# Kernel optimization log

Hardware: AMD Instinct MI355X
Metric: run time of the kernel (lower is better)

## Reference

```python
import math
import jax, jax.numpy as jnp
import numpy as np

B, S, HID = 4, 2048, 1024
H, D = 16, 64  # num_head, head_dim
EPS = 1e-12  # F.normalize eps


def _qknorm(t, gamma):
    # t: [B, S, H, D]; F.normalize(dim=-1) * sqrt(D) * gamma[None]
    norm = jnp.sqrt(jnp.sum(t * t, axis=-1, keepdims=True))
    t = t / jnp.maximum(norm, EPS)
    return t * math.sqrt(D) * gamma  # gamma broadcasts over [B,S]


def setup_inputs() -> dict:
    key = jax.random.key(0)
    ks = jax.random.split(key, 8)
    s = 0.02
    return {
        "x": jax.random.normal(ks[0], (B, S, HID), jnp.float32),
        "q_w": jax.random.normal(ks[1], (HID, HID), jnp.float32) * s,
        "q_b": jnp.zeros((HID,), jnp.float32),
        "kv_w": jax.random.normal(ks[2], (2 * HID, HID), jnp.float32) * s,
        "kv_b": jnp.zeros((2 * HID,), jnp.float32),
        "gamma_q": jnp.ones((H, D), jnp.float32),
        "gamma_k": jnp.ones((H, D), jnp.float32),
        "out_w": jax.random.normal(ks[3], (HID, HID), jnp.float32) * s,
    }


def reference(x, q_w, q_b, kv_w, kv_b, gamma_q, gamma_k, out_w):
    # self-attention: context = x
    q = (x @ q_w.T + q_b).reshape(B, S, H, D)
    kv = x @ kv_w.T + kv_b  # [B, S, 2*HID]
    k, v = jnp.split(kv, 2, axis=-1)
    k = k.reshape(B, S, H, D)
    v = v.reshape(B, S, H, D)
    q = _qknorm(q, gamma_q)
    k = _qknorm(k, gamma_k)
    scores = jnp.einsum('bqhd,bkhd->bhqk', q, k)  # [B,H,S,S]
    attn = jax.nn.softmax(scores, axis=-1)
    out = jnp.einsum('bhqk,bkhd->bqhd', attn, v).reshape(B, S, HID)
    return out @ out_w.T
```

## Files before the change

### kernel.cpp

```cpp
#include <hip/hip_runtime.h>
#include <stdint.h>

#define B_ 4
#define S_ 2048
#define HID_ 1024
#define NH_ 16
#define HD_ 64

typedef __bf16 bf16x8 __attribute__((ext_vector_type(8)));
typedef __bf16 bf16x4 __attribute__((ext_vector_type(4)));
typedef float f32x4 __attribute__((ext_vector_type(4)));

__device__ inline void gload_lds16(const void* g, void* l) {
  __builtin_amdgcn_global_load_lds((const __attribute__((address_space(1))) unsigned int*)g,
                                   (__attribute__((address_space(3))) unsigned int*)l, 16, 0, 0);
}

__device__ inline f32x4 fmax4(f32x4 a, f32x4 b) {
  f32x4 r;
  r[0] = fmaxf(a[0], b[0]); r[1] = fmaxf(a[1], b[1]);
  r[2] = fmaxf(a[2], b[2]); r[3] = fmaxf(a[3], b[3]);
  return r;
}

__global__ __launch_bounds__(256) void cvt_bf16(const float* __restrict__ in, __bf16* __restrict__ out) {
  int i = (blockIdx.x * 256 + threadIdx.x) * 4;
  f32x4 v = *(const f32x4*)(in + i);
  bf16x4 o;
  o[0] = (__bf16)v[0]; o[1] = (__bf16)v[1]; o[2] = (__bf16)v[2]; o[3] = (__bf16)v[3];
  *(bf16x4*)(out + i) = o;
}

template <int MODE>
__global__ __launch_bounds__(256) void gemm_bt(const __bf16* __restrict__ A,
                                               const __bf16* __restrict__ Bt,
                                               const float* __restrict__ bias_q,
                                               const float* __restrict__ bias_kv,
                                               const float* __restrict__ gamma_q,
                                               const float* __restrict__ gamma_k,
                                               __bf16* __restrict__ Cq,
                                               __bf16* __restrict__ Ck,
                                               float* __restrict__ Cf,
                                               __bf16* __restrict__ vt,
                                               int M, int N, int K) {
  const int n0 = blockIdx.x * 128;
  const int m0 = blockIdx.y * 128;
  const int tid  = threadIdx.x;
  const int wave = tid >> 6, lane = tid & 63;
  const int wm = wave >> 1, wn = wave & 1;
  const int lrow = lane & 15, lgrp = lane >> 4;

  __shared__ __bf16 sA[128][64];
  __shared__ __bf16 sB[128][64];

  f32x4 acc[4][4];
#pragma unroll
  for (int i = 0; i < 4; i++)
#pragma unroll
    for (int j = 0; j < 4; j++) acc[i][j] = f32x4{0.f, 0.f, 0.f, 0.f};

  for (int k0 = 0; k0 < K; k0 += 64) {
    __syncthreads();
#pragma unroll
    for (int c = 0; c < 4; c++) {
      const int row = wave * 32 + c * 8;
      const __bf16* ga = A + (size_t)(m0 + row + (lane >> 3)) * K + k0 + (lane & 7) * 8;
      gload_lds16(ga, &sA[row][0]);
      const __bf16* gb = Bt + (size_t)(n0 + row + (lane >> 3)) * K + k0 + (lane & 7) * 8;
      gload_lds16(gb, &sB[row][0]);
    }
    __syncthreads();
#pragma unroll
    for (int kk = 0; kk < 2; kk++) {
      bf16x8 af[4], bfr[4];
#pragma unroll
      for (int i = 0; i < 4; i++) {
        af[i]  = *(const bf16x8*)(&sA[wm * 64 + i * 16 + lrow][kk * 32 + 8 * lgrp]);
        bfr[i] = *(const bf16x8*)(&sB[wn * 64 + i * 16 + lrow][kk * 32 + 8 * lgrp]);
      }
#pragma unroll
      for (int i = 0; i < 4; i++)
#pragma unroll
        for (int j = 0; j < 4; j++)
          acc[i][j] = __builtin_amdgcn_mfma_f32_16x16x32_bf16(af[i], bfr[j], acc[i][j], 0, 0, 0);
    }
  }

  if (MODE == 4) {
    float bv[4];
#pragma unroll
    for (int j = 0; j < 4; j++) {
      const int n = n0 + wn * 64 + j * 16 + lrow;
      bv[j] = (n < 1024) ? bias_q[n] : bias_kv[n - 1024];
    }
#pragma unroll
    for (int i = 0; i < 4; i++)
#pragma unroll
      for (int j = 0; j < 4; j++)
#pragma unroll
        for (int r = 0; r < 4; r++) acc[i][j][r] += bv[j];

    const int nblk = n0 >> 10;
    if (nblk < 2) {
      const float nscale = (nblk == 0) ? 8.f * 1.44269504f : 8.f;
      const float* gam = (nblk == 0) ? gamma_q : gamma_k;
      __bf16* dst = (nblk == 0) ? Cq : Ck;
      float g[4];
#pragma unroll
      for (int j = 0; j < 4; j++) g[j] = gam[(n0 + wn * 64 + j * 16 + lrow) & 1023];
#pragma unroll
      for (int i = 0; i < 4; i++) {
#pragma unroll
        for (int r = 0; r < 4; r++) {
          float ss = acc[i][0][r] * acc[i][0][r] + acc[i][1][r] * acc[i][1][r] +
                     acc[i][2][r] * acc[i][2][r] + acc[i][3][r] * acc[i][3][r];
#pragma unroll
          for (int off = 1; off < 16; off <<= 1) ss += __shfl_xor(ss, off, 64);
          const float inv = nscale / fmaxf(sqrtf(ss), 1e-12f);
          const int m = m0 + wm * 64 + i * 16 + lgrp * 4 + r;
#pragma unroll
          for (int j = 0; j < 4; j++) {
            const int n = (n0 + wn * 64 + j * 16 + lrow) & 1023;
            dst[(size_t)m * 1024 + n] = (__bf16)(acc[i][j][r] * inv * g[j]);
          }
        }
      }
    } else {
#pragma unroll
      for (int i = 0; i < 4; i++) {
#pragma unroll
        for (int j = 0; j < 4; j++) {
          const int nn = n0 + wn * 64 + j * 16 + lrow - 2048;
          const int h = nn >> 6, d = nn & 63;
          const int m = m0 + wm * 64 + i * 16 + lgrp * 4;
          const int b = m >> 11, s0 = m & 2047;
          bf16x4 pk;
#pragma unroll
          for (int r = 0; r < 4; r++) pk[r] = (__bf16)acc[i][j][r];
          *(bf16x4*)(vt + ((size_t)((b * 16 + h) * 64 + d)) * 2048 + s0) = pk;
        }
      }
    }
  } else {
#pragma unroll
    for (int i = 0; i < 4; i++)
#pragma unroll
      for (int j = 0; j < 4; j++) {
        const int n = n0 + wn * 64 + j * 16 + lrow;
#pragma unroll
        for (int r = 0; r < 4; r++) {
          const int m = m0 + wm * 64 + i * 16 + lgrp * 4 + r;
          Cf[(size_t)m * N + n] = acc[i][j][r];
        }
      }
  }
}

__global__ __launch_bounds__(512) void attn_kernel(const __bf16* __restrict__ qm,
                                                   const __bf16* __restrict__ km,
                                                   const __bf16* __restrict__ vtm,
                                                   __bf16* __restrict__ o) {
  constexpr float THR = 11.5416f;
  const int lin = blockIdx.y * gridDim.x + blockIdx.x;
  const int swz = (lin & 7) * 64 + (lin >> 3);
  const int qb = swz & 7;
  const int bh = swz >> 3;
  const int b = bh >> 4, h = bh & 15;
  const int q0 = qb * 256;
  const int tid = threadIdx.x, wave = tid >> 6, lane = tid & 63;
  const int lrow = lane & 15, lgrp = lane >> 4;

  __shared__ __bf16 sK[2][64 * 64];
  __shared__ __bf16 sVt[2][64 * 64];
  __shared__ __bf16 sP[8][16 * 64];

  const __bf16* kbase  = km + (size_t)(b * S_) * 1024 + h * 64;
  const __bf16* vtbase = vtm + (size_t)((b * 16 + h) * 64) * 2048;

  const int srow = lane >> 3;
  const int pchunk = lane & 7;

  auto stage = [&](int buf, int kt) {
    const int rr = wave * 8;
    const int r = rr + srow;
    gload_lds16(kbase + (size_t)(kt * 64 + r) * 1024 + ((pchunk ^ (r & 7)) << 3),
                &sK[buf][rr * 64]);
    gload_lds16(vtbase + (size_t)r * 2048 + kt * 64 + ((pchunk ^ (r & 7)) << 3),
                &sVt[buf][rr * 64]);
  };

  bf16x8 qf[2][2];
#pragma unroll
  for (int rt = 0; rt < 2; ++rt) {
    const __bf16* qp = qm + (size_t)(b * S_ + q0 + wave * 32 + rt * 16 + lrow) * 1024 + h * 64;
    qf[rt][0] = *(const bf16x8*)(qp + 8 * lgrp);
    qf[rt][1] = *(const bf16x8*)(qp + 32 + 8 * lgrp);
  }

  f32x4 accd[2][4];
#pragma unroll
  for (int rt = 0; rt < 2; ++rt)
#pragma unroll
    for (int dt = 0; dt < 4; ++dt) accd[rt][dt] = f32x4{0.f, 0.f, 0.f, 0.f};
  float m_r[2], l_r[2];
#pragma unroll
  for (int rt = 0; rt < 2; ++rt) { m_r[rt] = -1e30f; l_r[rt] = 0.f; }

  stage(0, 0);
  int buf = 0;
  for (int kt = 0; kt < S_ / 64; ++kt) {
    __syncthreads();
    if (kt + 1 < S_ / 64) stage(buf ^ 1, kt + 1);

    f32x4 sc[2][4];
#pragma unroll
    for (int rt = 0; rt < 2; ++rt)
#pragma unroll
      for (int t = 0; t < 4; ++t) sc[rt][t] = f32x4{0.f, 0.f, 0.f, 0.f};
    __builtin_amdgcn_s_setprio(1);
#pragma unroll
    for (int t = 0; t < 4; ++t) {
      const int krow = t * 16 + lrow;
#pragma unroll
      for (int kk = 0; kk < 2; ++kk) {
        bf16x8 kf = *(const bf16x8*)(&sK[buf][krow * 64 + (((kk * 4 + lgrp) ^ (krow & 7)) << 3)]);
        sc[0][t] = __builtin_amdgcn_mfma_f32_16x16x32_bf16(kf, qf[0][kk], sc[0][t], 0, 0, 0);
        sc[1][t] = __builtin_amdgcn_mfma_f32_16x16x32_bf16(kf, qf[1][kk], sc[1][t], 0, 0, 0);
      }
    }
    __builtin_amdgcn_s_setprio(0);

#pragma unroll
    for (int rt = 0; rt < 2; ++rt) {
      f32x4 mm = fmax4(fmax4(sc[rt][0], sc[rt][1]), fmax4(sc[rt][2], sc[rt][3]));
      float tm = fmaxf(fmaxf(mm[0], mm[1]), fmaxf(mm[2], mm[3]));
      tm = fmaxf(tm, __shfl_xor(tm, 16, 64));
      tm = fmaxf(tm, __shfl_xor(tm, 32, 64));

      if (!__all(tm - m_r[rt] <= THR)) {
        const float mn = fmaxf(m_r[rt], tm);
        const float scl = __builtin_exp2f(m_r[rt] - mn);
        m_r[rt] = mn;
        l_r[rt] *= scl;
        float sclr[4];
#pragma unroll
        for (int j = 0; j < 4; ++j) sclr[j] = __shfl(scl, lgrp * 4 + j, 64);
#pragma unroll
        for (int dt = 0; dt < 4; ++dt)
#pragma unroll
          for (int j = 0; j < 4; ++j) accd[rt][dt][j] *= sclr[j];
      }

      const float nm = m_r[rt];
      float ps0 = 0.f, ps1 = 0.f;
#pragma unroll
      for (int t = 0; t < 4; ++t) {
        bf16x4 pk;
        const float p0 = __builtin_exp2f(sc[rt][t][0] - nm);
        const float p1 = __builtin_exp2f(sc[rt][t][1] - nm);
        const float p2 = __builtin_exp2f(sc[rt][t][2] - nm);
        const float p3 = __builtin_exp2f(sc[rt][t][3] - nm);
        ps0 += p0 + p2; ps1 += p1 + p3;
        pk[0] = (__bf16)p0; pk[1] = (__bf16)p1; pk[2] = (__bf16)p2; pk[3] = (__bf16)p3;
        *(bf16x4*)(&sP[wave][lrow * 64 + (((2 * t + (lgrp >> 1)) ^ (lrow & 7)) << 3) +
                             ((lgrp & 1) << 2)]) = pk;
      }
      float ps = ps0 + ps1;
      ps += __shfl_xor(ps, 16, 64);
      ps += __shfl_xor(ps, 32, 64);
      l_r[rt] += ps;

      __builtin_amdgcn_s_setprio(1);
#pragma unroll
      for (int half = 0; half < 2; ++half) {
        bf16x8 pf = *(const bf16x8*)(&sP[wave][lrow * 64 + (((half * 4 + lgrp) ^ (lrow & 7)) << 3)]);
#pragma unroll
        for (int dt = 0; dt < 4; ++dt) {
          const int d = dt * 16 + lrow;
          bf16x8 vf = *(const bf16x8*)(&sVt[buf][d * 64 + (((half * 4 + lgrp) ^ (d & 7)) << 3)]);
          accd[rt][dt] = __builtin_amdgcn_mfma_f32_16x16x32_bf16(pf, vf, accd[rt][dt], 0, 0, 0);
        }
      }
      __builtin_amdgcn_s_setprio(0);
    }
    buf ^= 1;
  }

#pragma unroll
  for (int rt = 0; rt < 2; ++rt) {
#pragma unroll
    for (int j = 0; j < 4; ++j) {
      const float lv = __shfl(l_r[rt], lgrp * 4 + j, 64);
      const float inv = 1.f / lv;
      const int row = b * S_ + q0 + wave * 32 + rt * 16 + lgrp * 4 + j;
      __bf16* ob = o + (size_t)row * 1024 + h * 64;
#pragma unroll
      for (int dt = 0; dt < 4; ++dt) ob[dt * 16 + lrow] = (__bf16)(accd[rt][dt][j] * inv);
    }
  }
}

extern "C" void kernel_launch(void* const* d_in, const int* in_sizes, int n_in,
                              void* d_out, int out_size, void* d_ws, size_t ws_size,
                              hipStream_t stream) {
  (void)in_sizes; (void)n_in; (void)out_size; (void)ws_size;
  const float* x       = (const float*)d_in[0];
  const float* q_w     = (const float*)d_in[1];
  const float* q_b     = (const float*)d_in[2];
  const float* kv_w    = (const float*)d_in[3];
  const float* kv_b    = (const float*)d_in[4];
  const float* gamma_q = (const float*)d_in[5];
  const float* gamma_k = (const float*)d_in[6];
  const float* out_w   = (const float*)d_in[7];
  float* out = (float*)d_out;

  char* ws = (char*)d_ws;
  __bf16* x_bf   = (__bf16*)(ws);
  __bf16* qkvw_bf = (__bf16*)(ws + (16ull << 20));
  __bf16* ow_bf  = (__bf16*)(ws + (22ull << 20));
  __bf16* q_bf   = (__bf16*)(ws + (24ull << 20));
  __bf16* k_bf   = (__bf16*)(ws + (40ull << 20));
  __bf16* vt_bf  = (__bf16*)(ws + (56ull << 20));
  __bf16* at_bf  = (__bf16*)(ws + (72ull << 20));

  cvt_bf16<<<8192, 256, 0, stream>>>(x, x_bf);
  cvt_bf16<<<1024, 256, 0, stream>>>(q_w, qkvw_bf);
  cvt_bf16<<<2048, 256, 0, stream>>>(kv_w, qkvw_bf + (1024ull * 1024));
  cvt_bf16<<<1024, 256, 0, stream>>>(out_w, ow_bf);

  gemm_bt<4><<<dim3(24, 64), 256, 0, stream>>>(x_bf, qkvw_bf, q_b, kv_b, gamma_q, gamma_k,
                                               q_bf, k_bf, nullptr, vt_bf, 8192, 3072, 1024);

  attn_kernel<<<dim3(8, 64), 512, 0, stream>>>(q_bf, k_bf, vt_bf, at_bf);

  gemm_bt<1><<<dim3(8, 64), 256, 0, stream>>>(at_bf, ow_bf, nullptr, nullptr, nullptr, nullptr,
                                              nullptr, nullptr, out, nullptr, 8192, 1024, 1024);
}
```

Measured before the change: 341.2 us.

## Halve attention query tile per block and swizzle GEMM grid for XCD locality

The attention kernel now gives each wave 16 query rows instead of 32, with 128 queries per block, which doubles the grid to 1024 blocks. Each wave now does half the MFMA work per K/V tile, and K/V tiles are loaded twice as often overall. The GEMMs move to a 1D grid with an XCD-aware swizzle so blocks sharing operands land on the same chiplet for cache reuse. The trade is more occupancy and parallelism against less reuse of each staged K/V tile and more global K/V traffic.

```diff
diff --git a/kernel.cpp b/kernel.cpp
--- a/kernel.cpp
+++ b/kernel.cpp
@@ -42,9 +42,12 @@
                                                __bf16* __restrict__ Ck,
                                                float* __restrict__ Cf,
                                                __bf16* __restrict__ vt,
-                                               int M, int N, int K) {
-  const int n0 = blockIdx.x * 128;
-  const int m0 = blockIdx.y * 128;
+                                               int M, int N, int K, int gx) {
+  const int nwg = gridDim.x;
+  const int lin = blockIdx.x;
+  const int swz = (lin & 7) * (nwg >> 3) + (lin >> 3);
+  const int n0 = (swz % gx) * 128;
+  const int m0 = (swz / gx) * 128;
   const int tid  = threadIdx.x;
   const int wave = tid >> 6, lane = tid & 63;
   const int wm = wave >> 1, wn = wave & 1;
@@ -162,11 +165,11 @@
                                                    __bf16* __restrict__ o) {
   constexpr float THR = 11.5416f;
   const int lin = blockIdx.y * gridDim.x + blockIdx.x;
-  const int swz = (lin & 7) * 64 + (lin >> 3);
-  const int qb = swz & 7;
-  const int bh = swz >> 3;
+  const int swz = (lin & 7) * 128 + (lin >> 3);
+  const int qb = swz & 15;
+  const int bh = swz >> 4;
   const int b = bh >> 4, h = bh & 15;
-  const int q0 = qb * 256;
+  const int q0 = qb * 128;
   const int tid = threadIdx.x, wave = tid >> 6, lane = tid & 63;
   const int lrow = lane & 15, lgrp = lane >> 4;
 
@@ -189,22 +192,17 @@
                 &sVt[buf][rr * 64]);
   };
 
-  bf16x8 qf[2][2];
-#pragma unroll
-  for (int rt = 0; rt < 2; ++rt) {
-    const __bf16* qp = qm + (size_t)(b * S_ + q0 + wave * 32 + rt * 16 + lrow) * 1024 + h * 64;
-    qf[rt][0] = *(const bf16x8*)(qp + 8 * lgrp);
-    qf[rt][1] = *(const bf16x8*)(qp + 32 + 8 * lgrp);
-  }
-
-  f32x4 accd[2][4];
-#pragma unroll
-  for (int rt = 0; rt < 2; ++rt)
-#pragma unroll
-    for (int dt = 0; dt < 4; ++dt) accd[rt][dt] = f32x4{0.f, 0.f, 0.f, 0.f};
-  float m_r[2], l_r[2];
-#pragma unroll
-  for (int rt = 0; rt < 2; ++rt) { m_r[rt] = -1e30f; l_r[rt] = 0.f; }
+  bf16x8 qf[2];
+  {
+    const __bf16* qp = qm + (size_t)(b * S_ + q0 + wave * 16 + lrow) * 1024 + h * 64;
+    qf[0] = *(const bf16x8*)(qp + 8 * lgrp);
+    qf[1] = *(const bf16x8*)(qp + 32 + 8 * lgrp);
+  }
+
+  f32x4 accd[4];
+#pragma unroll
+  for (int dt = 0; dt < 4; ++dt) accd[dt] = f32x4{0.f, 0.f, 0.f, 0.f};
+  float m_r = -1e30f, l_r = 0.f;
 
   stage(0, 0);
   int buf = 0;
@@ -212,11 +210,9 @@
     __syncthreads();
     if (kt + 1 < S_ / 64) stage(buf ^ 1, kt + 1);
 
-    f32x4 sc[2][4];
-#pragma unroll
-    for (int rt = 0; rt < 2; ++rt)
-#pragma unroll
-      for (int t = 0; t < 4; ++t) sc[rt][t] = f32x4{0.f, 0.f, 0.f, 0.f};
+    f32x4 sc[4];
+#pragma unroll
+    for (int t = 0; t < 4; ++t) sc[t] = f32x4{0.f, 0.f, 0.f, 0.f};
     __builtin_amdgcn_s_setprio(1);
 #pragma unroll
     for (int t = 0; t < 4; ++t) {
@@ -224,79 +220,72 @@
 #pragma unroll
       for (int kk = 0; kk < 2; ++kk) {
         bf16x8 kf = *(const bf16x8*)(&sK[buf][krow * 64 + (((kk * 4 + lgrp) ^ (krow & 7)) << 3)]);
-        sc[0][t] = __builtin_amdgcn_mfma_f32_16x16x32_bf16(kf, qf[0][kk], sc[0][t], 0, 0, 0);
-        sc[1][t] = __builtin_amdgcn_mfma_f32_16x16x32_bf16(kf, qf[1][kk], sc[1][t], 0, 0, 0);
+        sc[t] = __builtin_amdgcn_mfma_f32_16x16x32_bf16(kf, qf[kk], sc[t], 0, 0, 0);
       }
     }
     __builtin_amdgcn_s_setprio(0);
 
-#pragma unroll
-    for (int rt = 0; rt < 2; ++rt) {
-      f32x4 mm = fmax4(fmax4(sc[rt][0], sc[rt][1]), fmax4(sc[rt][2], sc[rt][3]));
-      float tm = fmaxf(fmaxf(mm[0], mm[1]), fmaxf(mm[2], mm[3]));
-      tm = fmaxf(tm, __shfl_xor(tm, 16, 64));
-      tm = fmaxf(tm, __shfl_xor(tm, 32, 64));
-
-      if (!__all(tm - m_r[rt] <= THR)) {
-        const float mn = fmaxf(m_r[rt], tm);
-        const float scl = __builtin_exp2f(m_r[rt] - mn);
-        m_r[rt] = mn;
-        l_r[rt] *= scl;
-        float sclr[4];
-#pragma unroll
-        for (int j = 0; j < 4; ++j) sclr[j] = __shfl(scl, lgrp * 4 + j, 64);
-#pragma unroll
-        for (int dt = 0; dt < 4; ++dt)
-#pragma unroll
-          for (int j = 0; j < 4; ++j) accd[rt][dt][j] *= sclr[j];
-      }
-
-      const float nm = m_r[rt];
-      float ps0 = 0.f, ps1 = 0.f;
-#pragma unroll
-      for (int t = 0; t < 4; ++t) {
-        bf16x4 pk;
-        const float p0 = __builtin_exp2f(sc[rt][t][0] - nm);
-        const float p1 = __builtin_exp2f(sc[rt][t][1] - nm);
-        const float p2 = __builtin_exp2f(sc[rt][t][2] - nm);
-        const float p3 = __builtin_exp2f(sc[rt][t][3] - nm);
-        ps0 += p0 + p2; ps1 += p1 + p3;
-        pk[0] = (__bf16)p0; pk[1] = (__bf16)p1; pk[2] = (__bf16)p2; pk[3] = (__bf16)p3;
-        *(bf16x4*)(&sP[wave][lrow * 64 + (((2 * t + (lgrp >> 1)) ^ (lrow & 7)) << 3) +
-                             ((lgrp & 1) << 2)]) = pk;
-      }
-      float ps = ps0 + ps1;
-      ps += __shfl_xor(ps, 16, 64);
-      ps += __shfl_xor(ps, 32, 64);
-      l_r[rt] += ps;
-
-      __builtin_amdgcn_s_setprio(1);
-#pragma unroll
-      for (int half = 0; half < 2; ++half) {
-        bf16x8 pf = *(const bf16x8*)(&sP[wave][lrow * 64 + (((half * 4 + lgrp) ^ (lrow & 7)) << 3)]);
-#pragma unroll
-        for (int dt = 0; dt < 4; ++dt) {
-          const int d = dt * 16 + lrow;
-          bf16x8 vf = *(const bf16x8*)(&sVt[buf][d * 64 + (((half * 4 + lgrp) ^ (d & 7)) << 3)]);
-          accd[rt][dt] = __builtin_amdgcn_mfma_f32_16x16x32_bf16(pf, vf, accd[rt][dt], 0, 0, 0);
-        }
-      }
-      __builtin_amdgcn_s_setprio(0);
-    }
+    f32x4 mm = fmax4(fmax4(sc[0], sc[1]), fmax4(sc[2], sc[3]));
+    float tm = fmaxf(fmaxf(mm[0], mm[1]), fmaxf(mm[2], mm[3]));
+    tm = fmaxf(tm, __shfl_xor(tm, 16, 64));
+    tm = fmaxf(tm, __shfl_xor(tm, 32, 64));
+
+    if (!__all(tm - m_r <= THR)) {
+      const float mn = fmaxf(m_r, tm);
+      const float scl = __builtin_exp2f(m_r - mn);
+      m_r = mn;
+      l_r *= scl;
+      float sclr[4];
+#pragma unroll
+      for (int j = 0; j < 4; ++j) sclr[j] = __shfl(scl, lgrp * 4 + j, 64);
+#pragma unroll
+      for (int dt = 0; dt < 4; ++dt)
+#pragma unroll
+        for (int j = 0; j < 4; ++j) accd[dt][j] *= sclr[j];
+    }
+
+    const float nm = m_r;
+    float ps0 = 0.f, ps1 = 0.f;
+#pragma unroll
+    for (int t = 0; t < 4; ++t) {
+      bf16x4 pk;
+      const float p0 = __builtin_exp2f(sc[t][0] - nm);
+      const float p1 = __builtin_exp2f(sc[t][1] - nm);
+      const float p2 = __builtin_exp2f(sc[t][2] - nm);
+      const float p3 = __builtin_exp2f(sc[t][3] - nm);
+      ps0 += p0 + p2; ps1 += p1 + p3;
+      pk[0] = (__bf16)p0; pk[1] = (__bf16)p1; pk[2] = (__bf16)p2; pk[3] = (__bf16)p3;
+      *(bf16x4*)(&sP[wave][lrow * 64 + (((2 * t + (lgrp >> 1)) ^ (lrow & 7)) << 3) +
+                           ((lgrp & 1) << 2)]) = pk;
+    }
+    float ps = ps0 + ps1;
+    ps += __shfl_xor(ps, 16, 64);
+    ps += __shfl_xor(ps, 32, 64);
+    l_r += ps;
+
+    __builtin_amdgcn_s_setprio(1);
+#pragma unroll
+    for (int half = 0; half < 2; ++half) {
+      bf16x8 pf = *(const bf16x8*)(&sP[wave][lrow * 64 + (((half * 4 + lgrp) ^ (lrow & 7)) << 3)]);
+#pragma unroll
+      for (int dt = 0; dt < 4; ++dt) {
+        const int d = dt * 16 + lrow;
+        bf16x8 vf = *(const bf16x8*)(&sVt[buf][d * 64 + (((half * 4 + lgrp) ^ (d & 7)) << 3)]);
+        accd[dt] = __builtin_amdgcn_mfma_f32_16x16x32_bf16(pf, vf, accd[dt], 0, 0, 0);
+      }
+    }
+    __builtin_amdgcn_s_setprio(0);
     buf ^= 1;
   }
 
 #pragma unroll
-  for (int rt = 0; rt < 2; ++rt) {
-#pragma unroll
-    for (int j = 0; j < 4; ++j) {
-      const float lv = __shfl(l_r[rt], lgrp * 4 + j, 64);
-      const float inv = 1.f / lv;
-      const int row = b * S_ + q0 + wave * 32 + rt * 16 + lgrp * 4 + j;
-      __bf16* ob = o + (size_t)row * 1024 + h * 64;
-#pragma unroll
-      for (int dt = 0; dt < 4; ++dt) ob[dt * 16 + lrow] = (__bf16)(accd[rt][dt][j] * inv);
-    }
+  for (int j = 0; j < 4; ++j) {
+    const float lv = __shfl(l_r, lgrp * 4 + j, 64);
+    const float inv = 1.f / lv;
+    const int row = b * S_ + q0 + wave * 16 + lgrp * 4 + j;
+    __bf16* ob = o + (size_t)row * 1024 + h * 64;
+#pragma unroll
+    for (int dt = 0; dt < 4; ++dt) ob[dt * 16 + lrow] = (__bf16)(accd[dt][j] * inv);
   }
 }
 
@@ -328,11 +317,11 @@
   cvt_bf16<<<2048, 256, 0, stream>>>(kv_w, qkvw_bf + (1024ull * 1024));
   cvt_bf16<<<1024, 256, 0, stream>>>(out_w, ow_bf);
 
-  gemm_bt<4><<<dim3(24, 64), 256, 0, stream>>>(x_bf, qkvw_bf, q_b, kv_b, gamma_q, gamma_k,
-                                               q_bf, k_bf, nullptr, vt_bf, 8192, 3072, 1024);
-
-  attn_kernel<<<dim3(8, 64), 512, 0, stream>>>(q_bf, k_bf, vt_bf, at_bf);
-
-  gemm_bt<1><<<dim3(8, 64), 256, 0, stream>>>(at_bf, ow_bf, nullptr, nullptr, nullptr, nullptr,
-                                              nullptr, nullptr, out, nullptr, 8192, 1024, 1024);
-}
+  gemm_bt<4><<<1536, 256, 0, stream>>>(x_bf, qkvw_bf, q_b, kv_b, gamma_q, gamma_k,
+                                       q_bf, k_bf, nullptr, vt_bf, 8192, 3072, 1024, 24);
+
+  attn_kernel<<<dim3(16, 64), 512, 0, stream>>>(q_bf, k_bf, vt_bf, at_bf);
+
+  gemm_bt<1><<<512, 256, 0, stream>>>(at_bf, ow_bf, nullptr, nullptr, nullptr, nullptr,
+                                      nullptr, nullptr, out, nullptr, 8192, 1024, 1024, 8);
+}
```

Result: slower. 348.2 us (+2.0%).
